# Kernel optimization log

Hardware: AMD Instinct MI355X
Metric: run time of the kernel (lower is better)

## Reference

```python
import jax, jax.numpy as jnp
import numpy as np

N_NODES = 50000
N_EDGES = 800000
D_IN = 128
DIM = 128
N_LAYERS = 3
N_GRAPHS = 128


def setup_inputs() -> dict:
    key = jax.random.key(0)
    ks = jax.random.split(key, 10)
    x = jax.random.normal(ks[0], (N_NODES, D_IN), dtype=jnp.float32)
    edge_index = jax.random.randint(ks[1], (2, N_EDGES), 0, N_NODES, dtype=jnp.int64)
    batch = jnp.sort(jax.random.randint(ks[2], (N_NODES,), 0, N_GRAPHS, dtype=jnp.int64))
    def glorot(k, fan_in, fan_out):
        s = jnp.sqrt(6.0 / (fan_in + fan_out))
        return jax.random.uniform(k, (fan_in, fan_out), jnp.float32, -s, s)
    W0 = glorot(ks[3], D_IN, DIM)
    W1 = glorot(ks[4], DIM, DIM)
    W2 = glorot(ks[5], DIM, DIM)
    b0 = jnp.zeros((DIM,), jnp.float32)
    b1 = jnp.zeros((DIM,), jnp.float32)
    b2 = jnp.zeros((DIM,), jnp.float32)
    return {"x": x, "edge_index": edge_index, "batch": batch,
            "W0": W0, "b0": b0, "W1": W1, "b1": b1, "W2": W2, "b2": b2}


def _gcn_norm(edge_index, n_nodes):
    # add self-loops, then symmetric normalization (PyG gcn_norm)
    loops = jnp.arange(n_nodes, dtype=edge_index.dtype)
    src = jnp.concatenate([edge_index[0], loops])
    dst = jnp.concatenate([edge_index[1], loops])
    deg = jax.ops.segment_sum(jnp.ones_like(dst, dtype=jnp.float32), dst,
                              num_segments=n_nodes)
    dinv = jnp.where(deg > 0, jax.lax.rsqrt(deg), 0.0)
    norm = dinv[src] * dinv[dst]  # [E + N]
    return src, dst, norm


def _gcn_conv(x, W, b, src, dst, norm, n_nodes):
    h = x @ W                      # [N, dim]
    msgs = h[src] * norm[:, None]  # [E+N, dim] gather + edge scale
    out = jax.ops.segment_sum(msgs, dst, num_segments=n_nodes)  # scatter-add
    return out + b


def reference(x, edge_index, batch, W0, b0, W1, b1, W2, b2):
    n = x.shape[0]
    src, dst, norm = _gcn_norm(edge_index, n)
    Ws, bs = (W0, W1, W2), (b0, b1, b2)
    xs = []
    h = x
    for i in range(N_LAYERS):
        h = jax.nn.relu(_gcn_conv(h, Ws[i], bs[i], src, dst, norm, n))
        xs.append(h)
    # global mean pool per layer output
    counts = jax.ops.segment_sum(jnp.ones((n,), jnp.float32), batch,
                                 num_segments=N_GRAPHS)
    counts = jnp.maximum(counts, 1.0)[:, None]
    xpool = [jax.ops.segment_sum(h, batch, num_segments=N_GRAPHS) / counts
             for h in xs]
    return jnp.concatenate(xpool, axis=1), jnp.concatenate(xs, axis=1)
```

## Files before the change

### kernel.cpp

```cpp
#include <hip/hip_runtime.h>

#define NNODES 50000
#define NEDGES 800000
#define DIM 128
#define NGRAPHS 128
#define OUT1_STRIDE 384
#define OUT0_ELEMS (NGRAPHS * OUT1_STRIDE)
#define SCAN_CHUNK 512
#define ROWPAD 50048

typedef unsigned int uint;
typedef unsigned short ushort;
typedef short bf16x8 __attribute__((ext_vector_type(8)));
typedef float f32x4 __attribute__((ext_vector_type(4)));

union U4 { uint4 u; bf16x8 h; };

__device__ inline uint rne_bf16(float f) {
    uint b = __float_as_uint(f);
    return (b + 0x7fffu + ((b >> 16) & 1u)) >> 16;
}
__device__ inline uint pack_bf16(float lo, float hi) {
    return rne_bf16(lo) | (rne_bf16(hi) << 16);
}

__global__ void k_count(const int* __restrict__ dst, int* __restrict__ rowcnt,
                        int* __restrict__ rank, int E) {
    int e = blockIdx.x * blockDim.x + threadIdx.x;
    if (e < E) rank[e] = atomicAdd(&rowcnt[dst[e]], 1);
}

__global__ __launch_bounds__(512) void k_sum(const int* __restrict__ cnt,
                                             int* __restrict__ bsum,
                                             float* __restrict__ dinv, int n) {
    __shared__ int red[512];
    int t = threadIdx.x;
    int i = blockIdx.x * SCAN_CHUNK + t;
    int c = (i < n) ? cnt[i] : 0;
    if (i < n) dinv[i] = rsqrtf((float)c + 1.0f);
    red[t] = c;
    __syncthreads();
    for (int off = 256; off > 0; off >>= 1) {
        if (t < off) red[t] += red[t + off];
        __syncthreads();
    }
    if (t == 0) bsum[blockIdx.x] = red[0];
}

__global__ __launch_bounds__(128) void k_scanb(const int* __restrict__ bsum,
                                               int* __restrict__ boff, int nb) {
    __shared__ int s[128];
    int t = threadIdx.x;
    int v = (t < nb) ? bsum[t] : 0;
    s[t] = v;
    __syncthreads();
    for (int off = 1; off < 128; off <<= 1) {
        int u = (t >= off) ? s[t - off] : 0;
        __syncthreads();
        s[t] += u;
        __syncthreads();
    }
    boff[t] = s[t] - v;
    if (t == nb - 1) boff[nb] = s[t];
}

__global__ __launch_bounds__(512) void k_writeptr(const int* __restrict__ cnt,
                                                  const int* __restrict__ boff,
                                                  int* __restrict__ rowptr, int n) {
    __shared__ int s[512];
    int t = threadIdx.x;
    int i = blockIdx.x * SCAN_CHUNK + t;
    int v = (i < n) ? cnt[i] : 0;
    s[t] = v;
    __syncthreads();
    for (int off = 1; off < 512; off <<= 1) {
        int u = (t >= off) ? s[t - off] : 0;
        __syncthreads();
        s[t] += u;
        __syncthreads();
    }
    if (i < n) rowptr[i] = boff[blockIdx.x] + s[t] - v;
    if (i == n - 1) rowptr[n] = boff[blockIdx.x] + s[t];
}

__global__ void k_fill(const int* __restrict__ src, const int* __restrict__ dst,
                       const int* __restrict__ rowptr, const int* __restrict__ rank,
                       int* __restrict__ csr_src, int E) {
    int e = blockIdx.x * blockDim.x + threadIdx.x;
    if (e < E) {
        int d = dst[e];
        csr_src[rowptr[d] + rank[e]] = src[e];
    }
}

__global__ void k_bounds(const int* __restrict__ batch, int* __restrict__ start, int N) {
    int g = threadIdx.x;
    if (g > NGRAPHS) return;
    if (g == NGRAPHS) { start[g] = N; return; }
    int lo = 0, hi = N;
    while (lo < hi) {
        int mid = (lo + hi) >> 1;
        if (batch[mid] < g) lo = mid + 1; else hi = mid;
    }
    start[g] = lo;
}

__global__ void k_cast(const float* __restrict__ x, uint* __restrict__ xbf, int total) {
    int i = blockIdx.x * blockDim.x + threadIdx.x;
    if (i < total) {
        float2 v = ((const float2*)x)[i];
        xbf[i] = pack_bf16(v.x, v.y);
    }
}

__global__ __launch_bounds__(256) void k_wswz(const float* __restrict__ W0,
                                              const float* __restrict__ W1,
                                              const float* __restrict__ W2,
                                              uint* __restrict__ wz) {
    int layer = blockIdx.x >> 3;
    const float* W = (layer == 0) ? W0 : ((layer == 1) ? W1 : W2);
    int t = (blockIdx.x & 7) * 256 + threadIdx.x;
    int f = t >> 6, lane = t & 63;
    int kb = f >> 3, nt = f & 7;
    int q = lane >> 4, m = lane & 15;
    int col = nt * 16 + m;
    uint v[8];
#pragma unroll
    for (int j = 0; j < 8; ++j)
        v[j] = rne_bf16(W[(kb * 32 + q * 8 + j) * 128 + col]);
    uint4 o;
    o.x = v[0] | (v[1] << 16);
    o.y = v[2] | (v[3] << 16);
    o.z = v[4] | (v[5] << 16);
    o.w = v[6] | (v[7] << 16);
    ((uint4*)wz)[layer * 2048 + t] = o;
}

__global__ __launch_bounds__(256) void k_gemm(const uint* __restrict__ Abf,
                                              const uint* __restrict__ Wswz,
                                              uint* __restrict__ hb, int M) {
    __shared__ uint4 wsw[2048];
    __shared__ ushort cbuf[64 * 128];
    int tid = threadIdx.x;
#pragma unroll
    for (int i = 0; i < 8; ++i)
        wsw[i * 256 + tid] = ((const uint4*)Wswz)[i * 256 + tid];
    __syncthreads();
    int wave = tid >> 6, lane = tid & 63;
    int q = lane >> 4, m = lane & 15;
    int row0 = blockIdx.x * 64 + wave * 16;
    f32x4 zero = {0.0f, 0.0f, 0.0f, 0.0f};
    f32x4 acc[8];
#pragma unroll
    for (int i = 0; i < 8; ++i) acc[i] = zero;
    const uint4* Arow = (const uint4*)(Abf + (size_t)(row0 + m) * 64);
#pragma unroll
    for (int kb = 0; kb < 4; ++kb) {
        U4 a; a.u = Arow[kb * 4 + q];
#pragma unroll
        for (int nt = 0; nt < 8; ++nt) {
            U4 b; b.u = wsw[(kb * 8 + nt) * 64 + lane];
            acc[nt] = __builtin_amdgcn_mfma_f32_16x16x32_bf16(a.h, b.h, acc[nt], 0, 0, 0);
        }
    }
    ushort* cw = cbuf + wave * 16 * 128;
#pragma unroll
    for (int nt = 0; nt < 8; ++nt)
#pragma unroll
        for (int r = 0; r < 4; ++r)
            cw[(q * 4 + r) * 128 + nt * 16 + m] = (ushort)rne_bf16(acc[nt][r]);
    const uint4* cr4 = (const uint4*)cw;
#pragma unroll
    for (int i = 0; i < 4; ++i) {
        int c = i * 64 + lane;
        int grow = row0 + (c >> 4);
        uint4 v = cr4[c];
        if (grow < M) ((uint4*)hb)[(size_t)grow * 16 + (c & 15)] = v;
    }
}

__global__ __launch_bounds__(256) void k_agg(const uint* __restrict__ hb,
                                             const int* __restrict__ rowptr,
                                             const int* __restrict__ csr_src,
                                             const float* __restrict__ dinv,
                                             const float* __restrict__ bias,
                                             float* __restrict__ out1,
                                             uint* __restrict__ hbin,
                                             int N, int layer) {
    int wave = threadIdx.x >> 6;
    int lane = threadIdx.x & 63;
    int n = blockIdx.x * 4 + wave;
    if (n >= N) return;
    float din = dinv[n];
    uint u = hb[(size_t)n * 64 + lane];
    float ax = __uint_as_float(u << 16)         * din;
    float ay = __uint_as_float(u & 0xffff0000u) * din;
    int beg = rowptr[n], end = rowptr[n + 1];
    for (int base = beg; base < end; base += 64) {
        int cnt = min(64, end - base);
        int eidx = base + lane;
        int   smy = 0;
        float wmy = 0.0f;
        if (eidx < end) { smy = csr_src[eidx]; wmy = dinv[smy]; }
        int j = 0;
        for (; j + 4 <= cnt; j += 4) {
            int   s0 = __shfl(smy, j),     s1 = __shfl(smy, j + 1);
            int   s2 = __shfl(smy, j + 2), s3 = __shfl(smy, j + 3);
            float w0 = __shfl(wmy, j),     w1 = __shfl(wmy, j + 1);
            float w2 = __shfl(wmy, j + 2), w3 = __shfl(wmy, j + 3);
            uint u0 = hb[(size_t)s0 * 64 + lane];
            uint u1 = hb[(size_t)s1 * 64 + lane];
            uint u2 = hb[(size_t)s2 * 64 + lane];
            uint u3 = hb[(size_t)s3 * 64 + lane];
            ax += w0 * __uint_as_float(u0 << 16) + w1 * __uint_as_float(u1 << 16)
                + w2 * __uint_as_float(u2 << 16) + w3 * __uint_as_float(u3 << 16);
            ay += w0 * __uint_as_float(u0 & 0xffff0000u) + w1 * __uint_as_float(u1 & 0xffff0000u)
                + w2 * __uint_as_float(u2 & 0xffff0000u) + w3 * __uint_as_float(u3 & 0xffff0000u);
        }
        for (; j < cnt; ++j) {
            int   ss = __shfl(smy, j);
            float ww = __shfl(wmy, j);
            uint uu = hb[(size_t)ss * 64 + lane];
            ax += ww * __uint_as_float(uu << 16);
            ay += ww * __uint_as_float(uu & 0xffff0000u);
        }
    }
    float2 b = ((const float2*)bias)[lane];
    float ox = fmaxf(din * ax + b.x, 0.0f);
    float oy = fmaxf(din * ay + b.y, 0.0f);
    size_t o1 = (size_t)n * OUT1_STRIDE + layer * DIM + lane * 2;
    *(float2*)(out1 + o1) = make_float2(ox, oy);
    hbin[(size_t)n * 64 + lane] = pack_bf16(ox, oy);
}

__global__ __launch_bounds__(384) void k_pool(const float* __restrict__ out1,
                                              const int* __restrict__ start,
                                              float* __restrict__ out0) {
    int g = blockIdx.x;
    int c = threadIdx.x;
    int beg = start[g], end = start[g + 1];
    float acc = 0.0f;
    int i = beg;
    for (; i + 4 <= end; i += 4) {
        float a0 = out1[(size_t)(i    ) * OUT1_STRIDE + c];
        float a1 = out1[(size_t)(i + 1) * OUT1_STRIDE + c];
        float a2 = out1[(size_t)(i + 2) * OUT1_STRIDE + c];
        float a3 = out1[(size_t)(i + 3) * OUT1_STRIDE + c];
        acc += a0 + a1 + a2 + a3;
    }
    for (; i < end; ++i) acc += out1[(size_t)i * OUT1_STRIDE + c];
    float cnt = (float)(end - beg);
    out0[(size_t)g * OUT1_STRIDE + c] = acc / fmaxf(cnt, 1.0f);
}

extern "C" void kernel_launch(void* const* d_in, const int* in_sizes, int n_in,
                              void* d_out, int out_size, void* d_ws, size_t ws_size,
                              hipStream_t stream) {
    const float* x     = (const float*)d_in[0];
    const int*   ei    = (const int*)d_in[1];
    const int*   batch = (const int*)d_in[2];
    const float* W0 = (const float*)d_in[3];
    const float* b0 = (const float*)d_in[4];
    const float* W1 = (const float*)d_in[5];
    const float* b1 = (const float*)d_in[6];
    const float* W2 = (const float*)d_in[7];
    const float* b2 = (const float*)d_in[8];
    (void)n_in; (void)ws_size; (void)out_size;

    const int E = in_sizes[1] / 2;
    const int N = in_sizes[2];
    const int* src = ei;
    const int* dst = ei + E;

    char* ws = (char*)d_ws;
    uint*  hb       = (uint*)ws;  ws += (size_t)ROWPAD * 64 * 4;
    uint*  hbin     = (uint*)ws;  ws += (size_t)ROWPAD * 64 * 4;
    uint*  xbf      = (uint*)ws;  ws += (size_t)ROWPAD * 64 * 4;
    uint*  wz       = (uint*)ws;  ws += 3 * 8192 * 4;
    float* dinv     = (float*)ws; ws += 50016 * 4;
    int*   rowcnt   = (int*)ws;   ws += 50016 * 4;
    int*   rowptr   = (int*)ws;   ws += 50016 * 4;
    int*   rank     = (int*)ws;   ws += (size_t)NEDGES * 4;
    int*   csr_src  = (int*)ws;   ws += (size_t)NEDGES * 4;
    int*   gstart   = (int*)ws;   ws += 256 * 4;
    int*   bsum     = (int*)ws;   ws += 256 * 4;
    int*   boff     = (int*)ws;   ws += 256 * 4;

    float* out0 = (float*)d_out;
    float* out1 = (float*)d_out + OUT0_ELEMS;

    const int nb = (N + SCAN_CHUNK - 1) / SCAN_CHUNK;

    hipMemsetAsync(rowcnt, 0, (size_t)N * 4, stream);

    k_count   <<<(E + 255) / 256, 256, 0, stream>>>(dst, rowcnt, rank, E);
    k_sum     <<<nb, 512, 0, stream>>>(rowcnt, bsum, dinv, N);
    k_scanb   <<<1, 128, 0, stream>>>(bsum, boff, nb);
    k_writeptr<<<nb, 512, 0, stream>>>(rowcnt, boff, rowptr, N);
    k_fill    <<<(E + 255) / 256, 256, 0, stream>>>(src, dst, rowptr, rank, csr_src, E);
    k_bounds  <<<1, 256, 0, stream>>>(batch, gstart, N);
    k_cast    <<<(N * 64 + 255) / 256, 256, 0, stream>>>(x, xbf, N * 64);
    k_wswz    <<<24, 256, 0, stream>>>(W0, W1, W2, wz);

    const float* bs[3] = {b0, b1, b2};
    const int ngb = (N + 63) / 64;
    for (int l = 0; l < 3; ++l) {
        const uint* Ain = (l == 0) ? xbf : hbin;
        k_gemm<<<ngb, 256, 0, stream>>>(Ain, wz + l * 8192, hb, N);
        k_agg <<<(N + 3) / 4, 256, 0, stream>>>(hb, rowptr, csr_src, dinv,
                                                bs[l], out1, hbin, N, l);
    }
    k_pool<<<NGRAPHS, 384, 0, stream>>>(out1, gstart, out0);
}
```

Measured before the change: 349.2 us.

## Fuse bf16 cast into GEMM, drop hbin buffer, merge prep kernels

```diff
diff --git a/kernel.cpp b/kernel.cpp
--- a/kernel.cpp
+++ b/kernel.cpp
@@ -22,6 +22,37 @@
 }
 __device__ inline uint pack_bf16(float lo, float hi) {
     return rne_bf16(lo) | (rne_bf16(hi) << 16);
+}
+__device__ inline float blo(uint u) { return __uint_as_float(u << 16); }
+__device__ inline float bhi(uint u) { return __uint_as_float(u & 0xffff0000u); }
+
+__global__ __launch_bounds__(256) void k_pre(const float* __restrict__ W0,
+                                             const float* __restrict__ W1,
+                                             const float* __restrict__ W2,
+                                             uint* __restrict__ wz,
+                                             int* __restrict__ rowcnt, int N) {
+    if (blockIdx.x >= 24) {
+        int i = (blockIdx.x - 24) * 256 + threadIdx.x;
+        if (i < N) rowcnt[i] = 0;
+        return;
+    }
+    int layer = blockIdx.x >> 3;
+    const float* W = (layer == 0) ? W0 : ((layer == 1) ? W1 : W2);
+    int t = (blockIdx.x & 7) * 256 + threadIdx.x;
+    int f = t >> 6, lane = t & 63;
+    int kb = f >> 3, nt = f & 7;
+    int q = lane >> 4, m = lane & 15;
+    int col = nt * 16 + m;
+    uint v[8];
+#pragma unroll
+    for (int j = 0; j < 8; ++j)
+        v[j] = rne_bf16(W[(kb * 32 + q * 8 + j) * 128 + col]);
+    uint4 o;
+    o.x = v[0] | (v[1] << 16);
+    o.y = v[2] | (v[3] << 16);
+    o.z = v[4] | (v[5] << 16);
+    o.w = v[6] | (v[7] << 16);
+    ((uint4*)wz)[layer * 2048 + t] = o;
 }
 
 __global__ void k_count(const int* __restrict__ dst, int* __restrict__ rowcnt,
@@ -93,50 +124,7 @@
     }
 }
 
-__global__ void k_bounds(const int* __restrict__ batch, int* __restrict__ start, int N) {
-    int g = threadIdx.x;
-    if (g > NGRAPHS) return;
-    if (g == NGRAPHS) { start[g] = N; return; }
-    int lo = 0, hi = N;
-    while (lo < hi) {
-        int mid = (lo + hi) >> 1;
-        if (batch[mid] < g) lo = mid + 1; else hi = mid;
-    }
-    start[g] = lo;
-}
-
-__global__ void k_cast(const float* __restrict__ x, uint* __restrict__ xbf, int total) {
-    int i = blockIdx.x * blockDim.x + threadIdx.x;
-    if (i < total) {
-        float2 v = ((const float2*)x)[i];
-        xbf[i] = pack_bf16(v.x, v.y);
-    }
-}
-
-__global__ __launch_bounds__(256) void k_wswz(const float* __restrict__ W0,
-                                              const float* __restrict__ W1,
-                                              const float* __restrict__ W2,
-                                              uint* __restrict__ wz) {
-    int layer = blockIdx.x >> 3;
-    const float* W = (layer == 0) ? W0 : ((layer == 1) ? W1 : W2);
-    int t = (blockIdx.x & 7) * 256 + threadIdx.x;
-    int f = t >> 6, lane = t & 63;
-    int kb = f >> 3, nt = f & 7;
-    int q = lane >> 4, m = lane & 15;
-    int col = nt * 16 + m;
-    uint v[8];
-#pragma unroll
-    for (int j = 0; j < 8; ++j)
-        v[j] = rne_bf16(W[(kb * 32 + q * 8 + j) * 128 + col]);
-    uint4 o;
-    o.x = v[0] | (v[1] << 16);
-    o.y = v[2] | (v[3] << 16);
-    o.z = v[4] | (v[5] << 16);
-    o.w = v[6] | (v[7] << 16);
-    ((uint4*)wz)[layer * 2048 + t] = o;
-}
-
-__global__ __launch_bounds__(256) void k_gemm(const uint* __restrict__ Abf,
+__global__ __launch_bounds__(256) void k_gemm(const float* __restrict__ A, int lda,
                                               const uint* __restrict__ Wswz,
                                               uint* __restrict__ hb, int M) {
     __shared__ uint4 wsw[2048];
@@ -149,14 +137,21 @@
     int wave = tid >> 6, lane = tid & 63;
     int q = lane >> 4, m = lane & 15;
     int row0 = blockIdx.x * 64 + wave * 16;
+    int arow = min(row0 + m, M - 1);
+    const float* Ar = A + (size_t)arow * lda + q * 8;
     f32x4 zero = {0.0f, 0.0f, 0.0f, 0.0f};
     f32x4 acc[8];
 #pragma unroll
     for (int i = 0; i < 8; ++i) acc[i] = zero;
-    const uint4* Arow = (const uint4*)(Abf + (size_t)(row0 + m) * 64);
 #pragma unroll
     for (int kb = 0; kb < 4; ++kb) {
-        U4 a; a.u = Arow[kb * 4 + q];
+        float4 f0 = *(const float4*)(Ar + kb * 32);
+        float4 f1 = *(const float4*)(Ar + kb * 32 + 4);
+        U4 a;
+        a.u.x = pack_bf16(f0.x, f0.y);
+        a.u.y = pack_bf16(f0.z, f0.w);
+        a.u.z = pack_bf16(f1.x, f1.y);
+        a.u.w = pack_bf16(f1.z, f1.w);
 #pragma unroll
         for (int nt = 0; nt < 8; ++nt) {
             U4 b; b.u = wsw[(kb * 8 + nt) * 64 + lane];
@@ -185,7 +180,6 @@
                                              const float* __restrict__ dinv,
                                              const float* __restrict__ bias,
                                              float* __restrict__ out1,
-                                             uint* __restrict__ hbin,
                                              int N, int layer) {
     int wave = threadIdx.x >> 6;
     int lane = threadIdx.x & 63;
@@ -193,16 +187,37 @@
     if (n >= N) return;
     float din = dinv[n];
     uint u = hb[(size_t)n * 64 + lane];
-    float ax = __uint_as_float(u << 16)         * din;
-    float ay = __uint_as_float(u & 0xffff0000u) * din;
+    float ax = blo(u) * din;
+    float ay = bhi(u) * din;
     int beg = rowptr[n], end = rowptr[n + 1];
     for (int base = beg; base < end; base += 64) {
         int cnt = min(64, end - base);
         int eidx = base + lane;
-        int   smy = 0;
-        float wmy = 0.0f;
+        int smy = 0; float wmy = 0.0f;
         if (eidx < end) { smy = csr_src[eidx]; wmy = dinv[smy]; }
         int j = 0;
+        for (; j + 8 <= cnt; j += 8) {
+            int   s0 = __shfl(smy, j),     s1 = __shfl(smy, j + 1);
+            int   s2 = __shfl(smy, j + 2), s3 = __shfl(smy, j + 3);
+            int   s4 = __shfl(smy, j + 4), s5 = __shfl(smy, j + 5);
+            int   s6 = __shfl(smy, j + 6), s7 = __shfl(smy, j + 7);
+            float w0 = __shfl(wmy, j),     w1 = __shfl(wmy, j + 1);
+            float w2 = __shfl(wmy, j + 2), w3 = __shfl(wmy, j + 3);
+            float w4 = __shfl(wmy, j + 4), w5 = __shfl(wmy, j + 5);
+            float w6 = __shfl(wmy, j + 6), w7 = __shfl(wmy, j + 7);
+            uint u0 = hb[(size_t)s0 * 64 + lane];
+            uint u1 = hb[(size_t)s1 * 64 + lane];
+            uint u2 = hb[(size_t)s2 * 64 + lane];
+            uint u3 = hb[(size_t)s3 * 64 + lane];
+            uint u4 = hb[(size_t)s4 * 64 + lane];
+            uint u5 = hb[(size_t)s5 * 64 + lane];
+            uint u6 = hb[(size_t)s6 * 64 + lane];
+            uint u7 = hb[(size_t)s7 * 64 + lane];
+            ax += w0 * blo(u0) + w1 * blo(u1) + w2 * blo(u2) + w3 * blo(u3)
+                + w4 * blo(u4) + w5 * blo(u5) + w6 * blo(u6) + w7 * blo(u7);
+            ay += w0 * bhi(u0) + w1 * bhi(u1) + w2 * bhi(u2) + w3 * bhi(u3)
+                + w4 * bhi(u4) + w5 * bhi(u5) + w6 * bhi(u6) + w7 * bhi(u7);
+        }
         for (; j + 4 <= cnt; j += 4) {
             int   s0 = __shfl(smy, j),     s1 = __shfl(smy, j + 1);
             int   s2 = __shfl(smy, j + 2), s3 = __shfl(smy, j + 3);
@@ -212,17 +227,15 @@
             uint u1 = hb[(size_t)s1 * 64 + lane];
             uint u2 = hb[(size_t)s2 * 64 + lane];
             uint u3 = hb[(size_t)s3 * 64 + lane];
-            ax += w0 * __uint_as_float(u0 << 16) + w1 * __uint_as_float(u1 << 16)
-                + w2 * __uint_as_float(u2 << 16) + w3 * __uint_as_float(u3 << 16);
-            ay += w0 * __uint_as_float(u0 & 0xffff0000u) + w1 * __uint_as_float(u1 & 0xffff0000u)
-                + w2 * __uint_as_float(u2 & 0xffff0000u) + w3 * __uint_as_float(u3 & 0xffff0000u);
+            ax += w0 * blo(u0) + w1 * blo(u1) + w2 * blo(u2) + w3 * blo(u3);
+            ay += w0 * bhi(u0) + w1 * bhi(u1) + w2 * bhi(u2) + w3 * bhi(u3);
         }
         for (; j < cnt; ++j) {
             int   ss = __shfl(smy, j);
             float ww = __shfl(wmy, j);
             uint uu = hb[(size_t)ss * 64 + lane];
-            ax += ww * __uint_as_float(uu << 16);
-            ay += ww * __uint_as_float(uu & 0xffff0000u);
+            ax += ww * blo(uu);
+            ay += ww * bhi(uu);
         }
     }
     float2 b = ((const float2*)bias)[lane];
@@ -230,15 +243,19 @@
     float oy = fmaxf(din * ay + b.y, 0.0f);
     size_t o1 = (size_t)n * OUT1_STRIDE + layer * DIM + lane * 2;
     *(float2*)(out1 + o1) = make_float2(ox, oy);
-    hbin[(size_t)n * 64 + lane] = pack_bf16(ox, oy);
 }
 
 __global__ __launch_bounds__(384) void k_pool(const float* __restrict__ out1,
-                                              const int* __restrict__ start,
-                                              float* __restrict__ out0) {
+                                              const int* __restrict__ batch,
+                                              float* __restrict__ out0, int N) {
     int g = blockIdx.x;
+    int lo = 0, hi = N;
+    while (lo < hi) { int mid = (lo + hi) >> 1; if (batch[mid] < g) lo = mid + 1; else hi = mid; }
+    int beg = lo;
+    hi = N;
+    while (lo < hi) { int mid = (lo + hi) >> 1; if (batch[mid] < g + 1) lo = mid + 1; else hi = mid; }
+    int end = lo;
     int c = threadIdx.x;
-    int beg = start[g], end = start[g + 1];
     float acc = 0.0f;
     int i = beg;
     for (; i + 4 <= end; i += 4) {
@@ -274,41 +291,36 @@
 
     char* ws = (char*)d_ws;
     uint*  hb       = (uint*)ws;  ws += (size_t)ROWPAD * 64 * 4;
-    uint*  hbin     = (uint*)ws;  ws += (size_t)ROWPAD * 64 * 4;
-    uint*  xbf      = (uint*)ws;  ws += (size_t)ROWPAD * 64 * 4;
     uint*  wz       = (uint*)ws;  ws += 3 * 8192 * 4;
     float* dinv     = (float*)ws; ws += 50016 * 4;
     int*   rowcnt   = (int*)ws;   ws += 50016 * 4;
     int*   rowptr   = (int*)ws;   ws += 50016 * 4;
     int*   rank     = (int*)ws;   ws += (size_t)NEDGES * 4;
     int*   csr_src  = (int*)ws;   ws += (size_t)NEDGES * 4;
-    int*   gstart   = (int*)ws;   ws += 256 * 4;
     int*   bsum     = (int*)ws;   ws += 256 * 4;
     int*   boff     = (int*)ws;   ws += 256 * 4;
 
     float* out0 = (float*)d_out;
     float* out1 = (float*)d_out + OUT0_ELEMS;
 
-    const int nb = (N + SCAN_CHUNK - 1) / SCAN_CHUNK;
-
-    hipMemsetAsync(rowcnt, 0, (size_t)N * 4, stream);
-
+    const int nb  = (N + SCAN_CHUNK - 1) / SCAN_CHUNK;
+    const int nbz = 24 + (N + 255) / 256;
+
+    k_pre     <<<nbz, 256, 0, stream>>>(W0, W1, W2, wz, rowcnt, N);
     k_count   <<<(E + 255) / 256, 256, 0, stream>>>(dst, rowcnt, rank, E);
     k_sum     <<<nb, 512, 0, stream>>>(rowcnt, bsum, dinv, N);
     k_scanb   <<<1, 128, 0, stream>>>(bsum, boff, nb);
     k_writeptr<<<nb, 512, 0, stream>>>(rowcnt, boff, rowptr, N);
     k_fill    <<<(E + 255) / 256, 256, 0, stream>>>(src, dst, rowptr, rank, csr_src, E);
-    k_bounds  <<<1, 256, 0, stream>>>(batch, gstart, N);
-    k_cast    <<<(N * 64 + 255) / 256, 256, 0, stream>>>(x, xbf, N * 64);
-    k_wswz    <<<24, 256, 0, stream>>>(W0, W1, W2, wz);
 
     const float* bs[3] = {b0, b1, b2};
     const int ngb = (N + 63) / 64;
     for (int l = 0; l < 3; ++l) {
-        const uint* Ain = (l == 0) ? xbf : hbin;
-        k_gemm<<<ngb, 256, 0, stream>>>(Ain, wz + l * 8192, hb, N);
+        const float* Ain = (l == 0) ? x : (out1 + (size_t)(l - 1) * DIM);
+        int lda          = (l == 0) ? DIM : OUT1_STRIDE;
+        k_gemm<<<ngb, 256, 0, stream>>>(Ain, lda, wz + l * 8192, hb, N);
         k_agg <<<(N + 3) / 4, 256, 0, stream>>>(hb, rowptr, csr_src, dinv,
-                                                bs[l], out1, hbin, N, l);
-    }
-    k_pool<<<NGRAPHS, 384, 0, stream>>>(out1, gstart, out0);
-}
+                                                bs[l], out1, N, l);
+    }
+    k_pool<<<NGRAPHS, 384, 0, stream>>>(out1, batch, out0, N);
+}
```

New measurement: 329.8 us. -5.6%, faster.
